# Optimization experiments

Hardware: AMD Instinct MI355X
Metric: run time of the kernel (lower is better)

The kernel has to match this reference:

```python
import jax, jax.numpy as jnp
import numpy as np

D_THRESH = 0.5  # init arg `dist`


def setup_inputs() -> dict:
    key = jax.random.key(0)
    k1, k2 = jax.random.split(key)
    N, M, C = 20000, 25000, 3
    pointcloud = jax.random.uniform(k1, (N, C), dtype=jnp.float32)
    pointcloud_padding = jax.random.uniform(k2, (M, C), dtype=jnp.float32)
    return {"pointcloud": pointcloud, "pointcloud_padding": pointcloud_padding}


def reference(pointcloud, pointcloud_padding):
    # torch.cdist(padding, pointcloud): Euclidean distance matrix [M, N]
    # via the GEMM formulation ||a||^2 + ||b||^2 - 2 a.b (matches torch's path)
    a2 = jnp.sum(pointcloud_padding * pointcloud_padding, axis=1)[:, None]  # [M,1]
    b2 = jnp.sum(pointcloud * pointcloud, axis=1)[None, :]                  # [1,N]
    ab = pointcloud_padding @ pointcloud.T                                  # [M,N]
    dist = jnp.sqrt(jnp.maximum(a2 + b2 - 2.0 * ab, 0.0))                   # [M,N]
    # count neighbors within radius, per pointcloud point
    counts = jnp.sum(dist <= D_THRESH, axis=0).astype(jnp.int32)            # [N]
    out = counts.reshape(-1, 1)[: pointcloud.shape[0]]                      # [N,1]
    return out
```

## Files before the change

### kernel.cpp

```cpp
#include <hip/hip_runtime.h>

typedef short  bf16x8 __attribute__((ext_vector_type(8)));
typedef float  f32x16 __attribute__((ext_vector_type(16)));

#define JS      8
#define STREAMS (JS * 4)
#define JTPAD   STREAMS
#define TI      128

__device__ __forceinline__ unsigned short f2bf(float x) {
    unsigned u = __builtin_bit_cast(unsigned, x);
    u += 0x7FFF + ((u >> 16) & 1);
    return (unsigned short)(u >> 16);
}
__device__ __forceinline__ float bf2f(unsigned short h) {
    unsigned u = ((unsigned)h) << 16;
    return __builtin_bit_cast(float, u);
}

__global__ __launch_bounds__(256) void dens_pack_kernel(
    const float* __restrict__ pad, uint4* __restrict__ ws,
    int* __restrict__ out, int M, int mtot, int N)
{
    const int j = blockIdx.x * 256 + threadIdx.x;
    if (j < N) out[j] = 0;
    if (j >= mtot) return;

    float qx = 0.f, qy = 0.f, qz = 0.f;
    float negc = -1.0e6f;
    if (j < M) {
        qx = pad[3 * j]; qy = pad[3 * j + 1]; qz = pad[3 * j + 2];
        negc = 0.125f - 0.5f * (qx * qx + qy * qy + qz * qz);
    }
    const unsigned short xh = f2bf(qx), yh = f2bf(qy), zh = f2bf(qz);
    const unsigned short xl = f2bf(qx - bf2f(xh));
    const unsigned short yl = f2bf(qy - bf2f(yh));
    const unsigned short zl = f2bf(qz - bf2f(zh));
    const unsigned short ch = f2bf(negc);
    const unsigned short cl = f2bf(negc - bf2f(ch));

    uint4 p0, p1;
    p0.x = (unsigned)xh | ((unsigned)yh << 16);
    p0.y = (unsigned)zh | ((unsigned)xl << 16);
    p0.z = (unsigned)yl | ((unsigned)zl << 16);
    p0.w = (unsigned)xh | ((unsigned)yh << 16);
    p1.x = (unsigned)zh | ((unsigned)xl << 16);
    p1.y = (unsigned)yl | ((unsigned)zl << 16);
    p1.z = (unsigned)ch | ((unsigned)cl << 16);
    p1.w = 0;
    ws[j]        = p0;
    ws[mtot + j] = p1;
}

__device__ __forceinline__ void make_bfrag(const float* __restrict__ pc,
                                           int i, int N, int half,
                                           bf16x8& B, float& ha)
{
    float px = 0.f, py = 0.f, pz = 0.f;
    ha = 3.0e38f;
    if (i < N) {
        px = pc[3 * i]; py = pc[3 * i + 1]; pz = pc[3 * i + 2];
        ha = 0.5f * (px * px + py * py + pz * pz);
    }
    const short xh = (short)f2bf(px), yh = (short)f2bf(py), zh = (short)f2bf(pz);
    const short xl = (short)f2bf(px - bf2f((unsigned short)xh));
    const short yl = (short)f2bf(py - bf2f((unsigned short)yh));
    const short zl = (short)f2bf(pz - bf2f((unsigned short)zh));
    const short ONE = (short)0x3F80;
    const bf16x8 B0 = {xh, yh, zh, xh, yh, zh, xl, yl};
    const bf16x8 B1 = {zl, xl, yl, zl, ONE, ONE, 0, 0};
    B = half ? B1 : B0;
}

__global__ __launch_bounds__(256, 2) void dens_mfma_kernel(
    const float* __restrict__ pc,
    const char*  __restrict__ wsA,
    int* __restrict__ out,
    int N, int jt, int p1off)
{
    const int lane = threadIdx.x & 63;
    const int w    = threadIdx.x >> 6;
    const int n    = lane & 31;
    const int half = lane >> 5;

    const int ibase = blockIdx.x * TI;
    bf16x8 B0, B1, B2, B3; float ha0, ha1, ha2, ha3;
    make_bfrag(pc, ibase + n,      N, half, B0, ha0);
    make_bfrag(pc, ibase + 32 + n, N, half, B1, ha1);
    make_bfrag(pc, ibase + 64 + n, N, half, B2, ha2);
    make_bfrag(pc, ibase + 96 + n, N, half, B3, ha3);

    const int stream = blockIdx.y * 4 + w;
    const char* aptr = wsA + (half ? p1off : 0) + n * 16 + (size_t)stream * 512;

    f32x16 Z = {0.f};
    int c0 = 0, c1 = 0, c2 = 0, c3 = 0;

    bf16x8 A = *(const bf16x8*)aptr;

    for (int t = stream; t < jt; t += STREAMS) {
        const bf16x8 An = *(const bf16x8*)(aptr + STREAMS * 512);
        f32x16 s0, s1, s2, s3;
        asm("s_nop 1\n\t"
            "v_mfma_f32_32x32x16_bf16 %0, %4, %5, %9\n\t"
            "v_mfma_f32_32x32x16_bf16 %1, %4, %6, %9\n\t"
            "v_mfma_f32_32x32x16_bf16 %2, %4, %7, %9\n\t"
            "v_mfma_f32_32x32x16_bf16 %3, %4, %8, %9\n\t"
            "s_nop 7\n\t"
            "s_nop 7"
            : "=&v"(s0), "=&v"(s1), "=&v"(s2), "=&v"(s3)
            : "v"(A), "v"(B0), "v"(B1), "v"(B2), "v"(B3), "v"(Z));
        #pragma unroll
        for (int r = 0; r < 16; ++r) c0 += (s0[r] >= ha0);
        #pragma unroll
        for (int r = 0; r < 16; ++r) c1 += (s1[r] >= ha1);
        #pragma unroll
        for (int r = 0; r < 16; ++r) c2 += (s2[r] >= ha2);
        #pragma unroll
        for (int r = 0; r < 16; ++r) c3 += (s3[r] >= ha3);
        A = An;
        aptr += STREAMS * 512;
    }

    int g0 = c0 + __shfl_xor(c0, 32);
    int g1 = c1 + __shfl_xor(c1, 32);
    int g2 = c2 + __shfl_xor(c2, 32);
    int g3 = c3 + __shfl_xor(c3, 32);

    __shared__ int red[4][TI];
    if (lane < 32) {
        red[w][n]      = g0;
        red[w][n + 32] = g1;
        red[w][n + 64] = g2;
        red[w][n + 96] = g3;
    }
    __syncthreads();
    if (threadIdx.x < TI) {
        const int ii = ibase + threadIdx.x;
        if (ii < N) {
            const int s = red[0][threadIdx.x] + red[1][threadIdx.x] +
                          red[2][threadIdx.x] + red[3][threadIdx.x];
            atomicAdd(&out[ii], s);
        }
    }
}

extern "C" void kernel_launch(void* const* d_in, const int* in_sizes, int n_in,
                              void* d_out, int out_size, void* d_ws, size_t ws_size,
                              hipStream_t stream) {
    const float* pc  = (const float*)d_in[0];
    const float* pad = (const float*)d_in[1];
    int* out = (int*)d_out;

    const int N = in_sizes[0] / 3;
    const int M = in_sizes[1] / 3;
    const int jt   = (M + 31) / 32;
    const int jtp  = jt + JTPAD;
    const int mtot = jtp * 32;

    dens_pack_kernel<<<(mtot + 255) / 256, 256, 0, stream>>>(
        pad, (uint4*)d_ws, out, M, mtot, N);

    dim3 grid((N + TI - 1) / TI, JS);
    dens_mfma_kernel<<<grid, 256, 0, stream>>>(
        pc, (const char*)d_ws, out, N, jt, mtot * 16);
}
```

Before: 96.23 us.

## Hand-schedule MFMA loop in inline asm, interleaving compare-counts with matrix ops

Replaces the compiler-generated loop with a single inline-asm loop over a fixed visit count. The loop prefetches the next A fragment and interleaves the MFMA issues with v_cmp/v_addc count accumulation on earlier results, which removes the long s_nop stalls and shortens the per-element compare-and-add sequence. Tiles past jt are handled by padding the workspace to whole visits, where the padded rows carry a large negative constant so they never count. The change relies on hardcoded VGPRs and hand-tuned nop counts for MFMA result hazards, so a register clash or a wrong hazard wait could produce incorrect counts.

New measurement: 91.85 us. -4.5%, faster.

```diff
diff --git a/kernel.cpp b/kernel.cpp
--- a/kernel.cpp
+++ b/kernel.cpp
@@ -1,11 +1,9 @@
 #include <hip/hip_runtime.h>
 
 typedef short  bf16x8 __attribute__((ext_vector_type(8)));
-typedef float  f32x16 __attribute__((ext_vector_type(16)));
 
 #define JS      8
 #define STREAMS (JS * 4)
-#define JTPAD   STREAMS
 #define TI      128
 
 __device__ __forceinline__ unsigned short f2bf(float x) {
@@ -72,6 +70,12 @@
     B = half ? B1 : B0;
 }
 
+#define CONSUME(R, HA, CC) \
+    "v_cmp_le_f32 vcc, " HA ", " R "\n\t" \
+    "v_addc_co_u32 " CC ", vcc, 0, " CC ", vcc\n\t"
+#define CONS4(R0, R1, R2, R3, HA, CC) \
+    CONSUME(R0, HA, CC) CONSUME(R1, HA, CC) CONSUME(R2, HA, CC) CONSUME(R3, HA, CC)
+
 __global__ __launch_bounds__(256, 2) void dens_mfma_kernel(
     const float* __restrict__ pc,
     const char*  __restrict__ wsA,
@@ -91,36 +95,75 @@
     make_bfrag(pc, ibase + 96 + n, N, half, B3, ha3);
 
     const int stream = blockIdx.y * 4 + w;
-    const char* aptr = wsA + (half ? p1off : 0) + n * 16 + (size_t)stream * 512;
-
-    f32x16 Z = {0.f};
+    const unsigned long long a0 =
+        (unsigned long long)(wsA + (half ? p1off : 0) + n * 16 + (size_t)stream * 512);
+    const unsigned alo = (unsigned)a0;
+    const unsigned ahi = (unsigned)(a0 >> 32);
+
+    int visits = (jt + STREAMS - 1) / STREAMS;
     int c0 = 0, c1 = 0, c2 = 0, c3 = 0;
 
-    bf16x8 A = *(const bf16x8*)aptr;
-
-    for (int t = stream; t < jt; t += STREAMS) {
-        const bf16x8 An = *(const bf16x8*)(aptr + STREAMS * 512);
-        f32x16 s0, s1, s2, s3;
-        asm("s_nop 1\n\t"
-            "v_mfma_f32_32x32x16_bf16 %0, %4, %5, %9\n\t"
-            "v_mfma_f32_32x32x16_bf16 %1, %4, %6, %9\n\t"
-            "v_mfma_f32_32x32x16_bf16 %2, %4, %7, %9\n\t"
-            "v_mfma_f32_32x32x16_bf16 %3, %4, %8, %9\n\t"
-            "s_nop 7\n\t"
-            "s_nop 7"
-            : "=&v"(s0), "=&v"(s1), "=&v"(s2), "=&v"(s3)
-            : "v"(A), "v"(B0), "v"(B1), "v"(B2), "v"(B3), "v"(Z));
-        #pragma unroll
-        for (int r = 0; r < 16; ++r) c0 += (s0[r] >= ha0);
-        #pragma unroll
-        for (int r = 0; r < 16; ++r) c1 += (s1[r] >= ha1);
-        #pragma unroll
-        for (int r = 0; r < 16; ++r) c2 += (s2[r] >= ha2);
-        #pragma unroll
-        for (int r = 0; r < 16; ++r) c3 += (s3[r] >= ha3);
-        A = An;
-        aptr += STREAMS * 512;
-    }
+    asm volatile(
+        "v_mov_b32 v88, %13\n\t"
+        "v_mov_b32 v89, %14\n\t"
+        "v_mov_b32 v64, 0\n\t" "v_mov_b32 v65, 0\n\t"
+        "v_mov_b32 v66, 0\n\t" "v_mov_b32 v67, 0\n\t"
+        "v_mov_b32 v68, 0\n\t" "v_mov_b32 v69, 0\n\t"
+        "v_mov_b32 v70, 0\n\t" "v_mov_b32 v71, 0\n\t"
+        "v_mov_b32 v72, 0\n\t" "v_mov_b32 v73, 0\n\t"
+        "v_mov_b32 v74, 0\n\t" "v_mov_b32 v75, 0\n\t"
+        "v_mov_b32 v76, 0\n\t" "v_mov_b32 v77, 0\n\t"
+        "v_mov_b32 v78, 0\n\t" "v_mov_b32 v79, 0\n\t"
+        "global_load_dwordx4 v[84:87], v[88:89], off\n\t"
+        "v_add_co_u32 v88, vcc, 0x4000, v88\n\t"
+        "v_addc_co_u32 v89, vcc, 0, v89, vcc\n\t"
+        "Ldens%=:\n\t"
+        "s_waitcnt vmcnt(0)\n\t"
+        "v_mov_b32 v80, v84\n\t"
+        "v_mov_b32 v81, v85\n\t"
+        "v_mov_b32 v82, v86\n\t"
+        "v_mov_b32 v83, v87\n\t"
+        "global_load_dwordx4 v[84:87], v[88:89], off\n\t"
+        "v_add_co_u32 v88, vcc, 0x4000, v88\n\t"
+        "v_addc_co_u32 v89, vcc, 0, v89, vcc\n\t"
+        "v_mfma_f32_32x32x16_bf16 v[32:47], v[80:83], %5, v[64:79]\n\t"
+        "v_mfma_f32_32x32x16_bf16 v[48:63], v[80:83], %6, v[64:79]\n\t"
+        "s_nop 7\n\t"
+        "s_nop 2\n\t"
+        CONS4("v32","v33","v34","v35","%9","%0")
+        CONS4("v36","v37","v38","v39","%9","%0")
+        CONS4("v40","v41","v42","v43","%9","%0")
+        CONS4("v44","v45","v46","v47","%9","%0")
+        "v_mfma_f32_32x32x16_bf16 v[32:47], v[80:83], %7, v[64:79]\n\t"
+        CONS4("v48","v49","v50","v51","%10","%1")
+        CONS4("v52","v53","v54","v55","%10","%1")
+        CONS4("v56","v57","v58","v59","%10","%1")
+        CONS4("v60","v61","v62","v63","%10","%1")
+        "v_mfma_f32_32x32x16_bf16 v[48:63], v[80:83], %8, v[64:79]\n\t"
+        CONS4("v32","v33","v34","v35","%11","%2")
+        CONS4("v36","v37","v38","v39","%11","%2")
+        CONS4("v40","v41","v42","v43","%11","%2")
+        CONS4("v44","v45","v46","v47","%11","%2")
+        CONS4("v48","v49","v50","v51","%12","%3")
+        CONS4("v52","v53","v54","v55","%12","%3")
+        CONS4("v56","v57","v58","v59","%12","%3")
+        CONS4("v60","v61","v62","v63","%12","%3")
+        "s_sub_u32 %4, %4, 1\n\t"
+        "s_cmp_lg_u32 %4, 0\n\t"
+        "s_cbranch_scc1 Ldens%=\n\t"
+        : "+v"(c0), "+v"(c1), "+v"(c2), "+v"(c3), "+s"(visits)
+        : "v"(B0), "v"(B1), "v"(B2), "v"(B3),
+          "v"(ha0), "v"(ha1), "v"(ha2), "v"(ha3),
+          "v"(alo), "v"(ahi)
+        : "vcc", "scc", "memory",
+          "v32","v33","v34","v35","v36","v37","v38","v39",
+          "v40","v41","v42","v43","v44","v45","v46","v47",
+          "v48","v49","v50","v51","v52","v53","v54","v55",
+          "v56","v57","v58","v59","v60","v61","v62","v63",
+          "v64","v65","v66","v67","v68","v69","v70","v71",
+          "v72","v73","v74","v75","v76","v77","v78","v79",
+          "v80","v81","v82","v83","v84","v85","v86","v87",
+          "v88","v89");
 
     int g0 = c0 + __shfl_xor(c0, 32);
     int g1 = c1 + __shfl_xor(c1, 32);
@@ -154,9 +197,10 @@
 
     const int N = in_sizes[0] / 3;
     const int M = in_sizes[1] / 3;
-    const int jt   = (M + 31) / 32;
-    const int jtp  = jt + JTPAD;
-    const int mtot = jtp * 32;
+    const int jt     = (M + 31) / 32;
+    const int visits = (jt + STREAMS - 1) / STREAMS;
+    const int jtp    = (visits + 1) * STREAMS;
+    const int mtot   = jtp * 32;
 
     dens_pack_kernel<<<(mtot + 255) / 256, 256, 0, stream>>>(
         pad, (uint4*)d_ws, out, M, mtot, N);
```
